# Kernel tuning notes

Measured on AMD Instinct MI355X. Metric: run time of the kernel, lower is better.

The kernel has to match this reference:

```python
import math
import jax, jax.numpy as jnp
import numpy as np

S, B, D, MAX_LEN, P = 4096, 64, 256, 4096, 8


def _sinusoid_pe(max_len, dim):
    pos = np.arange(max_len, dtype=np.float32)[:, None]
    div = np.exp(np.arange(0, dim, 2, dtype=np.float32) * (-math.log(10000.0) / dim))
    pe = np.zeros((max_len, dim), dtype=np.float32)
    pe[:, 0::2] = np.sin(pos * div)
    pe[:, 1::2] = np.cos(pos * div)
    return jnp.asarray(pe)[:, None, :]  # [max_len, 1, dim]


def setup_inputs() -> dict:
    key = jax.random.key(0)
    k1, k2, k3 = jax.random.split(key, 3)
    x = jax.random.normal(k1, (S, B, D), dtype=jnp.float32)
    peak_positions = jax.random.randint(k2, (B, P), 0, S)  # int indices into seq axis
    pe = _sinusoid_pe(MAX_LEN, D)
    table = jax.random.normal(k3, (MAX_LEN, D), dtype=jnp.float32) * 0.02  # embedding weights
    return {"x": x, "peak_positions": peak_positions, "pe": pe, "table": table}


def reference(x, peak_positions, pe, table):
    seq_len, batch, dim = x.shape
    x = x + pe[:seq_len]  # broadcast [S,1,D] over batch
    # valid peaks: 0 <= p < seq_len; invalid contribute zero
    mask = (peak_positions >= 0) & (peak_positions < seq_len)  # [B,P]
    idx = jnp.where(mask, peak_positions, 0)  # safe gather index
    emb = table[idx] * mask[..., None].astype(x.dtype)  # [B,P,D]
    bidx = jnp.broadcast_to(jnp.arange(batch)[:, None], idx.shape)  # [B,P]
    # scatter-add embeddings at (peak_idx, batch) positions; duplicates accumulate
    peak_sum = jnp.zeros_like(x).at[idx, bidx].add(emb)
    return x + peak_sum
```

## Files before the change

kernel.cpp:

```cpp
#include <hip/hip_runtime.h>

#define S_LEN 4096
#define BATCH 64
#define DIM 256
#define NPEAK 8
#define TOTAL4 (S_LEN * BATCH * DIM / 4)

typedef float f32x4 __attribute__((ext_vector_type(4)));

__global__ __launch_bounds__(256) void fused_pe_peak_kernel(
    const f32x4* __restrict__ x,
    const int*   __restrict__ peaks,
    const f32x4* __restrict__ pe,
    const f32x4* __restrict__ table,
    f32x4* __restrict__ out)
{
    const int tid = blockIdx.x * blockDim.x + threadIdx.x;
    const int stride = gridDim.x * blockDim.x;
    const int b  = (tid >> 6) & (BATCH - 1);
    const int d4 = tid & (DIM / 4 - 1);

    int pk[NPEAK];
    #pragma unroll
    for (int j = 0; j < NPEAK; ++j) pk[j] = peaks[b * NPEAK + j];

    for (int i = tid; i < TOTAL4; i += stride) {
        const int s = i >> 12;
        f32x4 xv = __builtin_nontemporal_load(&x[i]);
        f32x4 pv = pe[(s << 6) + d4];
        f32x4 o = xv + pv;

        int cnt = 0;
        #pragma unroll
        for (int j = 0; j < NPEAK; ++j) cnt += (pk[j] == s) ? 1 : 0;
        if (cnt) {
            f32x4 tv = table[(s << 6) + d4];
            o += (float)cnt * tv;
        }
        __builtin_nontemporal_store(o, &out[i]);
    }
}

extern "C" void kernel_launch(void* const* d_in, const int* in_sizes, int n_in,
                              void* d_out, int out_size, void* d_ws, size_t ws_size,
                              hipStream_t stream) {
    const float* x     = (const float*)d_in[0];
    const int* peaks   = (const int*)d_in[1];
    const float* pe    = (const float*)d_in[2];
    const float* table = (const float*)d_in[3];

    fused_pe_peak_kernel<<<2048, 256, 0, stream>>>(
        (const f32x4*)x, peaks, (const f32x4*)pe, (const f32x4*)table,
        (f32x4*)d_out);
}
```

Baseline: 104.1 us.

## Assign one block per sequence row with shared-memory peak counts

The grid-stride kernel becomes one block per sequence position. Each block scans the peak list once into shared-memory per-batch counts, then streams the row's x values, adding pe loaded once per thread. Rows with no peaks take a fast path with no table load and no compare loop. This removes the per-element 8-way comparison. In exchange it adds a shared-memory setup phase and two barriers per block, and issues 4096 blocks instead of 2048 persistent ones.

```diff
diff --git a/kernel.cpp b/kernel.cpp
--- a/kernel.cpp
+++ b/kernel.cpp
@@ -4,7 +4,8 @@
 #define BATCH 64
 #define DIM 256
 #define NPEAK 8
-#define TOTAL4 (S_LEN * BATCH * DIM / 4)
+#define ROW4 (BATCH * DIM / 4)
+#define KITERS (ROW4 / 256)
 
 typedef float f32x4 __attribute__((ext_vector_type(4)));
 
@@ -15,29 +16,45 @@
     const f32x4* __restrict__ table,
     f32x4* __restrict__ out)
 {
-    const int tid = blockIdx.x * blockDim.x + threadIdx.x;
-    const int stride = gridDim.x * blockDim.x;
-    const int b  = (tid >> 6) & (BATCH - 1);
-    const int d4 = tid & (DIM / 4 - 1);
+    const int s = blockIdx.x;
+    const int t = threadIdx.x;
+    const int d4 = t & 63;
+    const int w  = t >> 6;
 
-    int pk[NPEAK];
+    __shared__ int cnt[BATCH];
+    __shared__ int anypeak;
+    if (t < BATCH) cnt[t] = 0;
+    if (t == 0) anypeak = 0;
+    __syncthreads();
     #pragma unroll
-    for (int j = 0; j < NPEAK; ++j) pk[j] = peaks[b * NPEAK + j];
+    for (int j = t; j < BATCH * NPEAK; j += 256) {
+        if (peaks[j] == s) {
+            atomicAdd(&cnt[j >> 3], 1);
+            anypeak = 1;
+        }
+    }
+    __syncthreads();
 
-    for (int i = tid; i < TOTAL4; i += stride) {
-        const int s = i >> 12;
-        f32x4 xv = __builtin_nontemporal_load(&x[i]);
-        f32x4 pv = pe[(s << 6) + d4];
-        f32x4 o = xv + pv;
+    const f32x4 pv = pe[(s << 6) + d4];
+    const size_t base = (size_t)s * ROW4;
 
-        int cnt = 0;
-        #pragma unroll
-        for (int j = 0; j < NPEAK; ++j) cnt += (pk[j] == s) ? 1 : 0;
-        if (cnt) {
-            f32x4 tv = table[(s << 6) + d4];
-            o += (float)cnt * tv;
+    if (!anypeak) {
+        #pragma unroll 1
+        for (int k = 0; k < KITERS; ++k) {
+            const size_t i = base + k * 256 + t;
+            f32x4 o = __builtin_nontemporal_load(&x[i]) + pv;
+            __builtin_nontemporal_store(o, &out[i]);
         }
-        __builtin_nontemporal_store(o, &out[i]);
+    } else {
+        const f32x4 tv = table[(s << 6) + d4];
+        #pragma unroll 1
+        for (int k = 0; k < KITERS; ++k) {
+            const size_t i = base + k * 256 + t;
+            f32x4 o = __builtin_nontemporal_load(&x[i]) + pv;
+            const int c = cnt[4 * k + w];
+            if (c) o += (float)c * tv;
+            __builtin_nontemporal_store(o, &out[i]);
+        }
     }
 }
 
@@ -49,7 +66,7 @@
     const float* pe    = (const float*)d_in[2];
     const float* table = (const float*)d_in[3];
 
-    fused_pe_peak_kernel<<<2048, 256, 0, stream>>>(
+    fused_pe_peak_kernel<<<S_LEN, 256, 0, stream>>>(
         (const f32x4*)x, peaks, (const f32x4*)pe, (const f32x4*)table,
         (f32x4*)d_out);
 }
```

Result: faster. 101.3 us, median of 2 (-2.6%).
